# Optimization experiments

Measured on AMD Instinct MI355X. Metric: run time of the kernel, lower is better.

## Reference

```python
import jax, jax.numpy as jnp
import numpy as np

B, S = 512, 512
VOCAB, E, H1, H2, NTAGS = 50000, 20, 30, 50, 45


def _xavier_scale(fan_in, fan_out):
    return float(np.sqrt(2.0 / (fan_in + fan_out)))


def setup_inputs() -> dict:
    key = jax.random.key(0)
    ks = jax.random.split(key, 32)
    n = lambda i, shape, s=1.0: jax.random.normal(ks[i], shape, dtype=jnp.float32) * s
    w = 0.1  # weight scale
    emb_f1 = n(0, (VOCAB, E), w).at[0].set(0.0)  # padding_idx=0
    emb_b1 = n(1, (VOCAB, E), w).at[0].set(0.0)
    xs1 = _xavier_scale(B, H1)
    xs2 = _xavier_scale(B, H2)
    inp = {
        "x": jax.random.randint(ks[2], (B, S), 0, VOCAB, dtype=jnp.int64),
        "emb_f1": emb_f1, "emb_b1": emb_b1,
        "h0_f1": n(3, (B, H1), xs1), "c0_f1": n(4, (B, H1), xs1),
        "Wih_f1": n(5, (4 * H1, E), w), "Whh_f1": n(6, (4 * H1, H1), w),
        "bih_f1": n(7, (4 * H1,), w), "bhh_f1": n(8, (4 * H1,), w),
        "h0_b1": n(9, (B, H1), xs1), "c0_b1": n(10, (B, H1), xs1),
        "Wih_b1": n(11, (4 * H1, E), w), "Whh_b1": n(12, (4 * H1, H1), w),
        "bih_b1": n(13, (4 * H1,), w), "bhh_b1": n(14, (4 * H1,), w),
        "h0_f2": n(15, (B, H2), xs2), "c0_f2": n(16, (B, H2), xs2),
        "Wih_f2": n(17, (4 * H2, 2 * H1), w), "Whh_f2": n(18, (4 * H2, H2), w),
        "bih_f2": n(19, (4 * H2,), w), "bhh_f2": n(20, (4 * H2,), w),
        "h0_b2": n(21, (B, H2), xs2), "c0_b2": n(22, (B, H2), xs2),
        "Wih_b2": n(23, (4 * H2, 2 * H1), w), "Whh_b2": n(24, (4 * H2, H2), w),
        "bih_b2": n(25, (4 * H2,), w), "bhh_b2": n(26, (4 * H2,), w),
        "lin_w": n(27, (NTAGS, 2 * H2), w), "lin_b": n(28, (NTAGS,), w),
    }
    return inp


def _run_lstm(seq, h0, c0, Wih, Whh, bih, bhh, forward):
    """PyTorch LSTMCell recurrence over seq (B,S,D). Replicates the original's
    quirks: backward dir appends hidden states in reversed time order, and the
    (S,B,H) stack is .view()-ed into (B,S,H) without transposing."""
    b, s, _ = seq.shape
    h = h0.shape[-1]
    xs = jnp.swapaxes(seq, 0, 1)  # (S,B,D)

    def step(carry, xt):
        hh, cc = carry
        g = xt @ Wih.T + bih + hh @ Whh.T + bhh  # (B, 4H), gate order i,f,g,o
        i, f, gg, o = jnp.split(g, 4, axis=-1)
        cc = jax.nn.sigmoid(f) * cc + jax.nn.sigmoid(i) * jnp.tanh(gg)
        hh = jax.nn.sigmoid(o) * jnp.tanh(cc)
        return (hh, cc), hh

    _, hs = jax.lax.scan(step, (h0, c0), xs, reverse=not forward)  # hs[i] ~ time i
    if not forward:
        hs = hs[::-1]  # torch appended in processing (reversed-time) order
    return hs.reshape(b, s, h)  # faithful buggy view (S,B,H) -> (B,S,H)


def reference(x, emb_f1, emb_b1,
              h0_f1, c0_f1, Wih_f1, Whh_f1, bih_f1, bhh_f1,
              h0_b1, c0_b1, Wih_b1, Whh_b1, bih_b1, bhh_b1,
              h0_f2, c0_f2, Wih_f2, Whh_f2, bih_f2, bhh_f2,
              h0_b2, c0_b2, Wih_b2, Whh_b2, bih_b2, bhh_b2,
              lin_w, lin_b):
    f1 = _run_lstm(emb_f1[x], h0_f1, c0_f1, Wih_f1, Whh_f1, bih_f1, bhh_f1, True)
    b1 = _run_lstm(emb_b1[x], h0_b1, c0_b1, Wih_b1, Whh_b1, bih_b1, bhh_b1, False)
    l1 = jnp.concatenate([f1, b1], axis=2)  # (B,S,2*H1)
    f2 = _run_lstm(l1, h0_f2, c0_f2, Wih_f2, Whh_f2, bih_f2, bhh_f2, True)
    b2 = _run_lstm(l1, h0_b2, c0_b2, Wih_b2, Whh_b2, bih_b2, bhh_b2, False)
    l2 = jnp.concatenate([f2, b2], axis=2)  # (B,S,2*H2)
    return l2 @ lin_w.T + lin_b  # (B,S,NTAGS)
```

## Files before the change

kernel.cpp:

```cpp
#include <hip/hip_runtime.h>
#include <hip/hip_bf16.h>

typedef __attribute__((ext_vector_type(8))) short short8;
typedef __attribute__((ext_vector_type(4))) float float4v;
typedef unsigned short ushort_t;

#define BB 512
#define SS 512
#define EE 20
#define H1C 30
#define H2C 50
#define NTC 45

#define BAR() asm volatile("s_waitcnt lgkmcnt(0)\n\ts_barrier" ::: "memory")
#define WFENCE() asm volatile("s_waitcnt lgkmcnt(0)" ::: "memory")

#if __has_builtin(__builtin_amdgcn_exp2f)
#define EXP2(x) __builtin_amdgcn_exp2f(x)
#else
#define EXP2(x) exp2f(x)
#endif
#if __has_builtin(__builtin_amdgcn_rcpf)
#define RCPF(x) __builtin_amdgcn_rcpf(x)
#else
#define RCPF(x) (1.0f / (x))
#endif

#define LOG2E 1.4426950408889634f

__device__ __forceinline__ float sigf(float v) {
    return RCPF(1.0f + EXP2(-1.4426950408889634f * v));
}
__device__ __forceinline__ float tanh_(float v) {
    return 2.0f * RCPF(1.0f + EXP2(-2.8853900817779268f * v)) - 1.0f;
}

__device__ __forceinline__ float lstm_act(float gi, float gf, float gg, float go, float& c) {
    gi = fmaxf(gi, -30.f); gf = fmaxf(gf, -30.f);
    gg = fmaxf(gg, -30.f); go = fmaxf(go, -30.f);
    float di = 1.f + EXP2(-gi), df = 1.f + EXP2(-gf);
    float dg = 1.f + EXP2(-gg), dO = 1.f + EXP2(-go);
    float r1 = RCPF(di * df), r2 = RCPF(dg * dO);
    float si = df * r1, sf = di * r1;
    float tg = 2.f * (dO * r2) - 1.f;
    float so = dg * r2;
    float cc = sf * c + si * tg;
    c = cc;
    float e = EXP2(-2.8853900817779268f * cc);
    return so * (2.f * RCPF(1.f + e) - 1.f);
}

__device__ __forceinline__ ushort_t f2bf(float f) {
    unsigned u = __float_as_uint(f);
    unsigned r = u + 0x7FFFu + ((u >> 16) & 1u);
    return (ushort_t)(r >> 16);
}
__device__ __forceinline__ float bf2f(ushort_t s) { return __uint_as_float(((unsigned)s) << 16); }

__device__ __forceinline__ float ldG(const void* p, int i, int f32) {
    if (f32) return ((const float*)p)[i];
    return bf2f(((const ushort_t*)p)[i]);
}
__device__ __forceinline__ int ldTok(const void* x, int i, int x64) {
    const int* xi = (const int*)x;
    return x64 ? xi[2 * i] : xi[i];
}

__global__ void detect_kernel(const void* bih, const void* x, int* flags) {
    if (threadIdx.x == 0 && blockIdx.x == 0) {
        const ushort_t* u = (const ushort_t*)bih;
        int isf = 0;
        for (int i = 0; i < 120; i++) {
            float v = fabsf(bf2f(u[i]));
            if (!(v < 16.0f)) isf = 1;
        }
        flags[0] = isf;
        const int* xi = (const int*)x;
        int orv = 0;
        for (int i = 1; i < 32; i += 2) orv |= xi[i];
        flags[1] = (orv == 0) ? 1 : 0;
    }
}

struct XR8 { uint4 a, b; };

__device__ __forceinline__ XR8 ldEmbRawQ(const void* emb, int tok, int quad, int f32v) {
    XR8 o;
    o.a.x = 0; o.a.y = 0; o.a.z = 0; o.a.w = 0; o.b = o.a;
    if (quad < 3) {
        if (f32v) {
            const float* p = (const float*)emb + (size_t)tok * EE + quad * 8;
            o.a = *(const uint4*)p;
            if (quad < 2) o.b = *(const uint4*)(p + 4);
        } else {
            const ushort_t* p = (const ushort_t*)emb + (size_t)tok * EE + quad * 8;
            uint2 v0 = *(const uint2*)p;
            o.a.x = v0.x; o.a.y = v0.y;
            if (quad < 2) { uint2 v1 = *(const uint2*)(p + 4); o.a.z = v1.x; o.a.w = v1.y; }
        }
    }
    return o;
}

__device__ __forceinline__ short8 buildB0(const XR8& e, int quad, int f32v) {
    short8 bx;
    if (f32v) {
        bx[0] = (short)f2bf(__uint_as_float(e.a.x)); bx[1] = (short)f2bf(__uint_as_float(e.a.y));
        bx[2] = (short)f2bf(__uint_as_float(e.a.z)); bx[3] = (short)f2bf(__uint_as_float(e.a.w));
        bx[4] = (short)f2bf(__uint_as_float(e.b.x)); bx[5] = (short)f2bf(__uint_as_float(e.b.y));
        bx[6] = (short)f2bf(__uint_as_float(e.b.z)); bx[7] = (short)f2bf(__uint_as_float(e.b.w));
    } else {
        bx[0] = (short)(e.a.x & 0xFFFF); bx[1] = (short)(e.a.x >> 16);
        bx[2] = (short)(e.a.y & 0xFFFF); bx[3] = (short)(e.a.y >> 16);
        bx[4] = (short)(e.a.z & 0xFFFF); bx[5] = (short)(e.a.z >> 16);
        bx[6] = (short)(e.a.w & 0xFFFF); bx[7] = (short)(e.a.w >> 16);
    }
    if (quad == 2) { bx[4] = (short)0x3F80; bx[5] = 0; bx[6] = 0; bx[7] = 0; }
    if (quad == 3) { bx[0]=0;bx[1]=0;bx[2]=0;bx[3]=0;bx[4]=0;bx[5]=0;bx[6]=0;bx[7]=0; }
    return bx;
}

__global__ __launch_bounds__(64, 1) void lstm1_kernel(
    const void* __restrict__ x,
    const void* __restrict__ emb_f, const void* __restrict__ emb_b,
    const void* __restrict__ h0_f, const void* __restrict__ c0_f,
    const void* __restrict__ Wih_f, const void* __restrict__ Whh_f,
    const void* __restrict__ bih_f, const void* __restrict__ bhh_f,
    const void* __restrict__ h0_b, const void* __restrict__ c0_b,
    const void* __restrict__ Wih_b, const void* __restrict__ Whh_b,
    const void* __restrict__ bih_b, const void* __restrict__ bhh_b,
    ushort_t* __restrict__ hsf, ushort_t* __restrict__ hsb,
    const int* __restrict__ flags)
{
    const int f32v = flags[0], x64 = flags[1];
    const int lane = threadIdx.x & 63, li = lane & 15, quad = lane >> 4;
    const int cg = blockIdx.x, dir = cg >> 5, j0 = (cg & 31) << 4;

    const void* emb = dir ? emb_b : emb_f;
    const void* h0  = dir ? h0_b  : h0_f;
    const void* c0  = dir ? c0_b  : c0_f;
    const void* Wih = dir ? Wih_b : Wih_f;
    const void* Whh = dir ? Whh_b : Whh_f;
    const void* bih = dir ? bih_b : bih_f;
    const void* bhh = dir ? bhh_b : bhh_f;
    ushort_t* hs = dir ? hsb : hsf;

    __shared__ int toks[16][SS];

    for (int idx = lane; idx < 16 * SS; idx += 64)
        toks[idx >> 9][idx & (SS - 1)] = ldTok(x, (j0 + (idx >> 9)) * SS + (idx & (SS - 1)), x64);

    const int gA = li & 3, nbase = li >> 2;
    const float sc = (gA == 2) ? 2.0f * LOG2E : LOG2E;
    short8 wxh[8], wxl[8], whh[8], whl[8];
    #pragma unroll
    for (int u = 0; u < 8; u++) {
        const int nn = u * 4 + nbase;
        const bool ok = nn < H1C;
        short8 xh, xl, hh, hl;
        #pragma unroll
        for (int j = 0; j < 8; j++) {
            const int k = quad * 8 + j;
            float wx = 0.f;
            if (ok) {
                if (k < EE) wx = ldG(Wih, (gA * H1C + nn) * EE + k, f32v);
                else if (k == 20) wx = ldG(bih, gA * H1C + nn, f32v) + ldG(bhh, gA * H1C + nn, f32v);
            }
            wx *= sc;
            ushort_t bx1 = f2bf(wx); xh[j] = (short)bx1; xl[j] = (short)f2bf(wx - bf2f(bx1));
            const int ns = j * 4 + quad;
            float wh = (ok && ns < H1C) ? sc * ldG(Whh, (gA * H1C + nn) * H1C + ns, f32v) : 0.f;
            ushort_t bh1 = f2bf(wh); hh[j] = (short)bh1; hl[j] = (short)f2bf(wh - bf2f(bh1));
        }
        wxh[u] = xh; wxl[u] = xl; whh[u] = hh; whl[u] = hl;
    }

    float creg[8];
    short8 b1;
    #pragma unroll
    for (int u = 0; u < 8; u++) {
        const int nn = u * 4 + quad;
        const bool ok = nn < H1C;
        creg[u] = ok ? ldG(c0, (j0 + li) * H1C + nn, f32v) : 0.f;
        b1[u] = ok ? (short)f2bf(ldG(h0, (j0 + li) * H1C + nn, f32v)) : (short)0;
    }

    const int t0 = dir ? SS - 1 : 0, dt = dir ? -1 : 1;

    WFENCE();

    int tkA = toks[li][t0 + dt * 3];
    int tkB = toks[li][t0 + dt * 4];
    XR8 e0r, e1r, e2r, e3r;
    float4v xacc[8];
    {
        int tk0 = toks[li][t0];
        int tk1 = toks[li][t0 + dt];
        int tk2 = toks[li][t0 + dt * 2];
        XR8 ecur = ldEmbRawQ(emb, tk0, quad, f32v);
        e1r = ldEmbRawQ(emb, tk1, quad, f32v);
        e2r = ldEmbRawQ(emb, tk2, quad, f32v);
        e0r = ecur; e3r = ecur;
        short8 bx = buildB0(ecur, quad, f32v);
        #pragma unroll
        for (int u = 0; u < 8; u++) {
            float4v a; a[0] = 0.f; a[1] = 0.f; a[2] = 0.f; a[3] = 0.f;
            a = __builtin_amdgcn_mfma_f32_16x16x32_bf16(wxh[u], bx, a, 0, 0, 0);
            a = __builtin_amdgcn_mfma_f32_16x16x32_bf16(wxl[u], bx, a, 0, 0, 0);
            xacc[u] = a;
        }
    }

    auto step = [&](int it, XR8& cons, XR8& fill, int& tk) {
        const int t = t0 + dt * it;
        float4v acc[8];
        #pragma unroll
        for (int u = 0; u < 8; u++) {
            float4v a = xacc[u];
            a = __builtin_amdgcn_mfma_f32_16x16x32_bf16(whh[u], b1, a, 0, 0, 0);
            a = __builtin_amdgcn_mfma_f32_16x16x32_bf16(whl[u], b1, a, 0, 0, 0);
            acc[u] = a;
        }
        if (it + 3 < SS) fill = ldEmbRawQ(emb, tk, quad, f32v);
        {
            int ti = it + 5; if (ti > SS - 1) ti = SS - 1;
            tk = toks[li][t0 + dt * ti];
        }
        short8 bx = buildB0(cons, quad, f32v);
        float4v xn[8];
        #pragma unroll
        for (int u = 0; u < 8; u++) {
            float4v a; a[0] = 0.f; a[1] = 0.f; a[2] = 0.f; a[3] = 0.f;
            a = __builtin_amdgcn_mfma_f32_16x16x32_bf16(wxh[u], bx, a, 0, 0, 0);
            a = __builtin_amdgcn_mfma_f32_16x16x32_bf16(wxl[u], bx, a, 0, 0, 0);
            xn[u] = a;
        }
        short8 hp;
        #pragma unroll
        for (int u = 0; u < 8; u++) {
            float hv = lstm_act(acc[u][0], acc[u][1], acc[u][2], acc[u][3], creg[u]);
            hp[u] = (short)f2bf(hv);
        }
        b1 = hp;
        *(short8*)&hs[((size_t)(j0 + li) * SS + t) * 32 + quad * 8] = hp;
        #pragma unroll
        for (int u = 0; u < 8; u++) xacc[u] = xn[u];
    };
    for (int it = 0; it < SS; it += 4) {
        step(it,     e1r, e3r, tkA);
        step(it + 1, e2r, e0r, tkB);
        step(it + 2, e3r, e1r, tkA);
        step(it + 3, e0r, e2r, tkB);
    }
}

__global__ __launch_bounds__(256) void lstm2_kernel(
    const ushort_t* __restrict__ hs1f, const ushort_t* __restrict__ hs1b,
    const void* __restrict__ h0_f, const void* __restrict__ c0_f,
    const void* __restrict__ Wih_f, const void* __restrict__ Whh_f,
    const void* __restrict__ bih_f, const void* __restrict__ bhh_f,
    const void* __restrict__ h0_b, const void* __restrict__ c0_b,
    const void* __restrict__ Wih_b, const void* __restrict__ Whh_b,
    const void* __restrict__ bih_b, const void* __restrict__ bhh_b,
    ushort_t* __restrict__ hsf, ushort_t* __restrict__ hsb,
    const int* __restrict__ flags)
{
    const int f32v = flags[0];
    const int wg = blockIdx.x, dir = wg >> 5, cb = (wg & 31) << 4, tid = threadIdx.x;
    const int wave = tid >> 6, lane = tid & 63, li = lane & 15, quad = lane >> 4;

    const void* h0  = dir ? h0_b  : h0_f;
    const void* c0  = dir ? c0_b  : c0_f;
    const void* Wih = dir ? Wih_b : Wih_f;
    const void* Whh = dir ? Whh_b : Whh_f;
    const void* bih = dir ? bih_b : bih_f;
    const void* bhh = dir ? bhh_b : bhh_f;
    ushort_t* hs = dir ? hsb : hsf;

    __shared__ __align__(16) ushort_t Af[2][4][64][8];
    for (int idx = tid; idx < 2 * 4 * 64 * 8; idx += 256) ((ushort_t*)Af)[idx] = 0;

    const int n = wave * 16 + li;
    const bool nok = n < H2C;

    short8 bhi[4][4], blo[4][4];
    float bias_g[4];
    #pragma unroll
    for (int g = 0; g < 4; g++) {
        const int wrow = g * H2C + n;
        bias_g[g] = nok ? (ldG(bih, wrow, f32v) + ldG(bhh, wrow, f32v)) : 0.f;
        #pragma unroll
        for (int kt = 0; kt < 4; kt++) {
            short8 hi, lo;
            #pragma unroll
            for (int j = 0; j < 8; j++) {
                int k = kt * 32 + quad * 8 + j;
                float w = 0.f;
                if (nok) {
                    if (k < 32) {
                        const int c = k, nn2 = (c & 7) * 4 + (c >> 3);
                        if (nn2 < H1C) w = ldG(Wih, wrow * (2 * H1C) + nn2, f32v);
                    } else if (k < 64) {
                        const int c = k - 32, nn2 = (c & 7) * 4 + (c >> 3);
                        if (nn2 < H1C) w = ldG(Wih, wrow * (2 * H1C) + H1C + nn2, f32v);
                    } else if (k < 64 + H2C) {
                        w = ldG(Whh, wrow * H2C + (k - 64), f32v);
                    }
                }
                ushort_t h = f2bf(w);
                hi[j] = (short)h;
                lo[j] = (short)f2bf(w - bf2f(h));
            }
            bhi[g][kt] = hi; blo[g][kt] = lo;
        }
    }

    const int kh = 64 + n;
    const int khk = kh >> 5, khg = (kh & 31) >> 3, khj = kh & 7;
    const int lrow = tid >> 4, k0 = (tid & 15) * 4;
    const int t0 = dir ? SS - 1 : 0, dt = dir ? -1 : 1;

    auto loadX = [&](int c) -> ushort4 {
        const int a = cb + lrow;
        if (k0 < 32)
            return *(const ushort4*)&hs1f[((size_t)c * SS + a) * 32 + k0];
        else
            return *(const ushort4*)&hs1b[((size_t)c * SS + (SS - 1 - a)) * 32 + (k0 - 32)];
    };

    __syncthreads();

    float creg[4];
    #pragma unroll
    for (int r = 0; r < 4; r++) {
        const int m = quad * 4 + r;
        creg[r] = nok ? ldG(c0, (cb + m) * H2C + n, f32v) : 0.f;
        ushort_t hb0 = nok ? f2bf(ldG(h0, (cb + m) * H2C + n, f32v)) : (ushort_t)0;
        Af[0][khk][khg * 16 + m][khj] = hb0;
    }
    {
        ushort4 xi = loadX(t0);
        const int kg = (k0 & 31) >> 3, kt = k0 >> 5, jb = k0 & 7;
        Af[0][kt][kg * 16 + lrow][jb + 0] = xi.x;
        Af[0][kt][kg * 16 + lrow][jb + 1] = xi.y;
        Af[0][kt][kg * 16 + lrow][jb + 2] = xi.z;
        Af[0][kt][kg * 16 + lrow][jb + 3] = xi.w;
    }
    ushort4 xA = loadX(t0 + dt), xB;
    __syncthreads();

    auto step = [&](int it, ushort4& xin, ushort4& xout) {
        const int c = t0 + dt * it;
        const int cur = it & 1, nxt = cur ^ 1;
        BAR();
        short8 af[4];
        #pragma unroll
        for (int kt = 0; kt < 4; kt++) af[kt] = *(const short8*)&Af[cur][kt][lane][0];
        if (it + 2 < SS) xout = loadX(c + 2 * dt);
        float4v acc[4];
        #pragma unroll
        for (int g = 0; g < 4; g++) {
            float4v a; a[0] = a[1] = a[2] = a[3] = bias_g[g];
            #pragma unroll
            for (int kt = 0; kt < 4; kt++) {
                a = __builtin_amdgcn_mfma_f32_16x16x32_bf16(af[kt], bhi[g][kt], a, 0, 0, 0);
                a = __builtin_amdgcn_mfma_f32_16x16x32_bf16(af[kt], blo[g][kt], a, 0, 0, 0);
            }
            acc[g] = a;
        }
        ushort_t hb[4];
        #pragma unroll
        for (int r = 0; r < 4; r++) {
            float gi = acc[0][r], gf = acc[1][r], gg = acc[2][r], go = acc[3][r];
            float cc = sigf(gf) * creg[r] + sigf(gi) * tanh_(gg);
            float h = sigf(go) * tanh_(cc);
            creg[r] = cc;
            hb[r] = nok ? f2bf(h) : (ushort_t)0;
        }
        ushort4 h4; h4.x = hb[0]; h4.y = hb[1]; h4.z = hb[2]; h4.w = hb[3];
        *(ushort4*)&hs[((size_t)c * 64 + n) * SS + cb + quad * 4] = h4;
        if (it + 1 < SS) {
            #pragma unroll
            for (int r = 0; r < 4; r++) Af[nxt][khk][khg * 16 + quad * 4 + r][khj] = hb[r];
            const int kg = (k0 & 31) >> 3, kt = k0 >> 5, jb = k0 & 7;
            Af[nxt][kt][kg * 16 + lrow][jb + 0] = xin.x;
            Af[nxt][kt][kg * 16 + lrow][jb + 1] = xin.y;
            Af[nxt][kt][kg * 16 + lrow][jb + 2] = xin.z;
            Af[nxt][kt][kg * 16 + lrow][jb + 3] = xin.w;
        }
    };
    for (int it = 0; it < SS; it += 2) { step(it, xA, xB); step(it + 1, xB, xA); }
}

__global__ __launch_bounds__(256) void lin_kernel(
    const ushort_t* __restrict__ hs2f, const ushort_t* __restrict__ hs2b,
    const void* __restrict__ lw, const void* __restrict__ lb,
    void* __restrict__ out, const int* __restrict__ flags)
{
    const int f32v = flags[0];
    const int tid = threadIdx.x, wave = tid >> 6, lane = tid & 63, li = lane & 15, quad = lane >> 4;

    __shared__ __align__(16) ushort_t Af[4][4][64][8];
    for (int idx = tid; idx < 4 * 4 * 64 * 8; idx += 256) ((ushort_t*)Af)[idx] = 0;

    short8 bhi[3][4], blo[3][4];
    float biasv[3];
    #pragma unroll
    for (int nt = 0; nt < 3; nt++) {
        const int nn = nt * 16 + li;
        const bool nok = nn < NTC;
        biasv[nt] = nok ? ldG(lb, nn, f32v) : 0.f;
        #pragma unroll
        for (int kt = 0; kt < 4; kt++) {
            short8 hi, lo;
            #pragma unroll
            for (int j = 0; j < 8; j++) {
                int k = kt * 32 + quad * 8 + j;
                float w = 0.f;
                if (nok) {
                    if (k < H2C) w = ldG(lw, nn * 100 + k, f32v);
                    else if (k >= 64 && k < 64 + H2C) w = ldG(lw, nn * 100 + 50 + (k - 64), f32v);
                }
                ushort_t h = f2bf(w);
                hi[j] = (short)h;
                lo[j] = (short)f2bf(w - bf2f(h));
            }
            bhi[nt][kt] = hi; blo[nt][kt] = lo;
        }
    }

    const int P0 = blockIdx.x * 64;
    const int i = P0 >> 9, j0 = P0 & 511;
    __syncthreads();
    for (int idx = tid; idx < 100 * 32; idx += 256) {
        const int kk = idx >> 5, pj = (idx & 31) * 2;
        unsigned v;
        int k;
        if (kk < H2C) {
            v = *(const unsigned*)&hs2f[((size_t)i * 64 + kk) * SS + j0 + pj];
            k = kk;
        } else {
            v = *(const unsigned*)&hs2b[((size_t)(SS - 1 - i) * 64 + (kk - H2C)) * SS + j0 + pj];
            k = 64 + (kk - H2C);
        }
        const int kt = k >> 5, kg = (k & 31) >> 3, j = k & 7;
        Af[pj >> 4][kt][kg * 16 + (pj & 15)][j] = (ushort_t)(v & 0xFFFF);
        Af[pj >> 4][kt][kg * 16 + ((pj + 1) & 15)][j] = (ushort_t)(v >> 16);
    }
    __syncthreads();

    short8 af[4];
    #pragma unroll
    for (int kt = 0; kt < 4; kt++) af[kt] = *(const short8*)&Af[wave][kt][lane][0];
    #pragma unroll
    for (int nt = 0; nt < 3; nt++) {
        float4v a; a[0] = a[1] = a[2] = a[3] = biasv[nt];
        #pragma unroll
        for (int kt = 0; kt < 4; kt++) {
            a = __builtin_amdgcn_mfma_f32_16x16x32_bf16(af[kt], bhi[nt][kt], a, 0, 0, 0);
            a = __builtin_amdgcn_mfma_f32_16x16x32_bf16(af[kt], blo[nt][kt], a, 0, 0, 0);
        }
        const int nn = nt * 16 + li;
        if (nn < NTC) {
            #pragma unroll
            for (int reg = 0; reg < 4; reg++) {
                const int prow = wave * 16 + quad * 4 + reg;
                const size_t op = (size_t)(P0 + prow) * NTC + nn;
                if (f32v) ((float*)out)[op] = a[reg];
                else      ((ushort_t*)out)[op] = f2bf(a[reg]);
            }
        }
    }
}

extern "C" void kernel_launch(void* const* d_in, const int* in_sizes, int n_in,
                              void* d_out, int out_size, void* d_ws, size_t ws_size,
                              hipStream_t stream)
{
    const void* x      = d_in[0];
    const void* emb_f1 = d_in[1];
    const void* emb_b1 = d_in[2];
    const void* h0_f1  = d_in[3];
    const void* c0_f1  = d_in[4];
    const void* Wih_f1 = d_in[5];
    const void* Whh_f1 = d_in[6];
    const void* bih_f1 = d_in[7];
    const void* bhh_f1 = d_in[8];
    const void* h0_b1  = d_in[9];
    const void* c0_b1  = d_in[10];
    const void* Wih_b1 = d_in[11];
    const void* Whh_b1 = d_in[12];
    const void* bih_b1 = d_in[13];
    const void* bhh_b1 = d_in[14];
    const void* h0_f2  = d_in[15];
    const void* c0_f2  = d_in[16];
    const void* Wih_f2 = d_in[17];
    const void* Whh_f2 = d_in[18];
    const void* bih_f2 = d_in[19];
    const void* bhh_f2 = d_in[20];
    const void* h0_b2  = d_in[21];
    const void* c0_b2  = d_in[22];
    const void* Wih_b2 = d_in[23];
    const void* Whh_b2 = d_in[24];
    const void* bih_b2 = d_in[25];
    const void* bhh_b2 = d_in[26];
    const void* lin_w  = d_in[27];
    const void* lin_b  = d_in[28];

    int* flags = (int*)d_ws;
    ushort_t* hs1f = (ushort_t*)((char*)d_ws + 256);
    ushort_t* hs1b = hs1f + (size_t)BB * SS * 32;
    ushort_t* hs2f = hs1b + (size_t)BB * SS * 32;
    ushort_t* hs2b = hs2f + (size_t)SS * 64 * BB;

    detect_kernel<<<1, 64, 0, stream>>>(bih_f1, x, flags);
    lstm1_kernel<<<64, 64, 0, stream>>>(x, emb_f1, emb_b1,
        h0_f1, c0_f1, Wih_f1, Whh_f1, bih_f1, bhh_f1,
        h0_b1, c0_b1, Wih_b1, Whh_b1, bih_b1, bhh_b1, hs1f, hs1b, flags);
    lstm2_kernel<<<64, 256, 0, stream>>>(hs1f, hs1b,
        h0_f2, c0_f2, Wih_f2, Whh_f2, bih_f2, bhh_f2,
        h0_b2, c0_b2, Wih_b2, Whh_b2, bih_b2, bhh_b2, hs2f, hs2b, flags);
    lin_kernel<<<(BB * SS) / 64, 256, 0, stream>>>(hs2f, hs2b, lin_w, lin_b, d_out, flags);
}
```

Baseline: 1.130 ms.

## Process two batch chunks per wave in layer-1 LSTM to interleave recurrences

Each layer-1 workgroup now handles two independent 16-row batch chunks instead of one, halving the grid to 32 single-wave blocks. The two recurrences are interleaved in the same step, so their MFMA chains and activations can hide each other's latency. Tokens are now read from global memory directly instead of being staged in shared memory. The cost is higher register pressure, fewer CUs in use, and more global token loads on the critical path.

New measurement: 1.703 ms. 1.51x slower.

```diff
diff --git a/kernel.cpp b/kernel.cpp
--- a/kernel.cpp
+++ b/kernel.cpp
@@ -13,7 +13,6 @@
 #define NTC 45
 
 #define BAR() asm volatile("s_waitcnt lgkmcnt(0)\n\ts_barrier" ::: "memory")
-#define WFENCE() asm volatile("s_waitcnt lgkmcnt(0)" ::: "memory")
 
 #if __has_builtin(__builtin_amdgcn_exp2f)
 #define EXP2(x) __builtin_amdgcn_exp2f(x)
@@ -120,7 +119,8 @@
     return bx;
 }
 
-__global__ __launch_bounds__(64, 1) void lstm1_kernel(
+__global__ __attribute__((amdgpu_waves_per_eu(1))) __launch_bounds__(64)
+void lstm1_kernel(
     const void* __restrict__ x,
     const void* __restrict__ emb_f, const void* __restrict__ emb_b,
     const void* __restrict__ h0_f, const void* __restrict__ c0_f,
@@ -134,7 +134,8 @@
 {
     const int f32v = flags[0], x64 = flags[1];
     const int lane = threadIdx.x & 63, li = lane & 15, quad = lane >> 4;
-    const int cg = blockIdx.x, dir = cg >> 5, j0 = (cg & 31) << 4;
+    const int wg = blockIdx.x, dir = wg >> 4, pr = wg & 15;
+    const int j0c[2] = { (pr * 2) << 4, (pr * 2 + 1) << 4 };
 
     const void* emb = dir ? emb_b : emb_f;
     const void* h0  = dir ? h0_b  : h0_f;
@@ -145,11 +146,6 @@
     const void* bhh = dir ? bhh_b : bhh_f;
     ushort_t* hs = dir ? hsb : hsf;
 
-    __shared__ int toks[16][SS];
-
-    for (int idx = lane; idx < 16 * SS; idx += 64)
-        toks[idx >> 9][idx & (SS - 1)] = ldTok(x, (j0 + (idx >> 9)) * SS + (idx & (SS - 1)), x64);
-
     const int gA = li & 3, nbase = li >> 2;
     const float sc = (gA == 2) ? 2.0f * LOG2E : LOG2E;
     short8 wxh[8], wxl[8], whh[8], whl[8];
@@ -175,82 +171,97 @@
         wxh[u] = xh; wxl[u] = xl; whh[u] = hh; whl[u] = hl;
     }
 
-    float creg[8];
-    short8 b1;
-    #pragma unroll
-    for (int u = 0; u < 8; u++) {
-        const int nn = u * 4 + quad;
-        const bool ok = nn < H1C;
-        creg[u] = ok ? ldG(c0, (j0 + li) * H1C + nn, f32v) : 0.f;
-        b1[u] = ok ? (short)f2bf(ldG(h0, (j0 + li) * H1C + nn, f32v)) : (short)0;
-    }
-
     const int t0 = dir ? SS - 1 : 0, dt = dir ? -1 : 1;
-
-    WFENCE();
-
-    int tkA = toks[li][t0 + dt * 3];
-    int tkB = toks[li][t0 + dt * 4];
-    XR8 e0r, e1r, e2r, e3r;
-    float4v xacc[8];
-    {
-        int tk0 = toks[li][t0];
-        int tk1 = toks[li][t0 + dt];
-        int tk2 = toks[li][t0 + dt * 2];
-        XR8 ecur = ldEmbRawQ(emb, tk0, quad, f32v);
-        e1r = ldEmbRawQ(emb, tk1, quad, f32v);
-        e2r = ldEmbRawQ(emb, tk2, quad, f32v);
-        e0r = ecur; e3r = ecur;
+    int rbase[2];
+    rbase[0] = (j0c[0] + li) * SS;
+    rbase[1] = (j0c[1] + li) * SS;
+
+    float creg[2][8];
+    short8 b1v[2];
+    XR8 er[2][4];
+    int tk[2][2];
+    float4v xacc[2][8];
+    #pragma unroll
+    for (int c = 0; c < 2; c++) {
+        const int jj = j0c[c];
+        #pragma unroll
+        for (int u = 0; u < 8; u++) {
+            const int nn = u * 4 + quad;
+            const bool ok = nn < H1C;
+            creg[c][u] = ok ? ldG(c0, (jj + li) * H1C + nn, f32v) : 0.f;
+            b1v[c][u] = ok ? (short)f2bf(ldG(h0, (jj + li) * H1C + nn, f32v)) : (short)0;
+        }
+        int tkp0 = ldTok(x, rbase[c] + t0, x64);
+        int tkp1 = ldTok(x, rbase[c] + t0 + dt, x64);
+        int tkp2 = ldTok(x, rbase[c] + t0 + 2 * dt, x64);
+        tk[c][0] = ldTok(x, rbase[c] + t0 + 3 * dt, x64);
+        tk[c][1] = ldTok(x, rbase[c] + t0 + 4 * dt, x64);
+        XR8 ecur = ldEmbRawQ(emb, tkp0, quad, f32v);
+        er[c][1] = ldEmbRawQ(emb, tkp1, quad, f32v);
+        er[c][2] = ldEmbRawQ(emb, tkp2, quad, f32v);
+        er[c][0] = ecur; er[c][3] = ecur;
         short8 bx = buildB0(ecur, quad, f32v);
         #pragma unroll
         for (int u = 0; u < 8; u++) {
             float4v a; a[0] = 0.f; a[1] = 0.f; a[2] = 0.f; a[3] = 0.f;
             a = __builtin_amdgcn_mfma_f32_16x16x32_bf16(wxh[u], bx, a, 0, 0, 0);
             a = __builtin_amdgcn_mfma_f32_16x16x32_bf16(wxl[u], bx, a, 0, 0, 0);
-            xacc[u] = a;
-        }
-    }
-
-    auto step = [&](int it, XR8& cons, XR8& fill, int& tk) {
+            xacc[c][u] = a;
+        }
+    }
+
+    auto step = [&](int it, int rc, int rf, int tp) {
         const int t = t0 + dt * it;
-        float4v acc[8];
+        float4v acc[2][8];
         #pragma unroll
         for (int u = 0; u < 8; u++) {
-            float4v a = xacc[u];
-            a = __builtin_amdgcn_mfma_f32_16x16x32_bf16(whh[u], b1, a, 0, 0, 0);
-            a = __builtin_amdgcn_mfma_f32_16x16x32_bf16(whl[u], b1, a, 0, 0, 0);
-            acc[u] = a;
-        }
-        if (it + 3 < SS) fill = ldEmbRawQ(emb, tk, quad, f32v);
-        {
+            #pragma unroll
+            for (int c = 0; c < 2; c++) {
+                float4v a = xacc[c][u];
+                a = __builtin_amdgcn_mfma_f32_16x16x32_bf16(whh[u], b1v[c], a, 0, 0, 0);
+                a = __builtin_amdgcn_mfma_f32_16x16x32_bf16(whl[u], b1v[c], a, 0, 0, 0);
+                acc[c][u] = a;
+            }
+        }
+        #pragma unroll
+        for (int c = 0; c < 2; c++) {
+            if (it + 3 < SS) er[c][rf] = ldEmbRawQ(emb, tk[c][tp], quad, f32v);
             int ti = it + 5; if (ti > SS - 1) ti = SS - 1;
-            tk = toks[li][t0 + dt * ti];
-        }
-        short8 bx = buildB0(cons, quad, f32v);
-        float4v xn[8];
-        #pragma unroll
-        for (int u = 0; u < 8; u++) {
-            float4v a; a[0] = 0.f; a[1] = 0.f; a[2] = 0.f; a[3] = 0.f;
-            a = __builtin_amdgcn_mfma_f32_16x16x32_bf16(wxh[u], bx, a, 0, 0, 0);
-            a = __builtin_amdgcn_mfma_f32_16x16x32_bf16(wxl[u], bx, a, 0, 0, 0);
-            xn[u] = a;
-        }
-        short8 hp;
-        #pragma unroll
-        for (int u = 0; u < 8; u++) {
-            float hv = lstm_act(acc[u][0], acc[u][1], acc[u][2], acc[u][3], creg[u]);
-            hp[u] = (short)f2bf(hv);
-        }
-        b1 = hp;
-        *(short8*)&hs[((size_t)(j0 + li) * SS + t) * 32 + quad * 8] = hp;
-        #pragma unroll
-        for (int u = 0; u < 8; u++) xacc[u] = xn[u];
+            tk[c][tp] = ldTok(x, rbase[c] + t0 + dt * ti, x64);
+        }
+        float4v xn[2][8];
+        #pragma unroll
+        for (int c = 0; c < 2; c++) {
+            short8 bx = buildB0(er[c][rc], quad, f32v);
+            #pragma unroll
+            for (int u = 0; u < 8; u++) {
+                float4v a; a[0] = 0.f; a[1] = 0.f; a[2] = 0.f; a[3] = 0.f;
+                a = __builtin_amdgcn_mfma_f32_16x16x32_bf16(wxh[u], bx, a, 0, 0, 0);
+                a = __builtin_amdgcn_mfma_f32_16x16x32_bf16(wxl[u], bx, a, 0, 0, 0);
+                xn[c][u] = a;
+            }
+        }
+        #pragma unroll
+        for (int c = 0; c < 2; c++) {
+            short8 hp;
+            #pragma unroll
+            for (int u = 0; u < 8; u++) {
+                float hv = lstm_act(acc[c][u][0], acc[c][u][1], acc[c][u][2], acc[c][u][3], creg[c][u]);
+                hp[u] = (short)f2bf(hv);
+            }
+            b1v[c] = hp;
+            *(short8*)&hs[((size_t)(j0c[c] + li) * SS + t) * 32 + quad * 8] = hp;
+        }
+        #pragma unroll
+        for (int c = 0; c < 2; c++)
+            #pragma unroll
+            for (int u = 0; u < 8; u++) xacc[c][u] = xn[c][u];
     };
     for (int it = 0; it < SS; it += 4) {
-        step(it,     e1r, e3r, tkA);
-        step(it + 1, e2r, e0r, tkB);
-        step(it + 2, e3r, e1r, tkA);
-        step(it + 3, e0r, e2r, tkB);
+        step(it,     1, 3, 0);
+        step(it + 1, 2, 0, 1);
+        step(it + 2, 3, 1, 0);
+        step(it + 3, 0, 2, 1);
     }
 }
 
@@ -514,7 +525,7 @@
     ushort_t* hs2b = hs2f + (size_t)SS * 64 * BB;
 
     detect_kernel<<<1, 64, 0, stream>>>(bih_f1, x, flags);
-    lstm1_kernel<<<64, 64, 0, stream>>>(x, emb_f1, emb_b1,
+    lstm1_kernel<<<32, 64, 0, stream>>>(x, emb_f1, emb_b1,
         h0_f1, c0_f1, Wih_f1, Whh_f1, bih_f1, bhh_f1,
         h0_b1, c0_b1, Wih_b1, Whh_b1, bih_b1, bhh_b1, hs1f, hs1b, flags);
     lstm2_kernel<<<64, 256, 0, stream>>>(hs1f, hs1b,
```

## Restructure layer-1 LSTM step: drop LDS token staging, fold x-projection into step

Applied to the files above, without the earlier changes.

Removes the shared-memory token table and loads tokens directly from global memory with a rotating 3-slot prefetch of token ids and embedding rows. The input projection MFMAs move out of the previous step's software pipeline and now feed the same accumulator chain as the recurrent MFMAs, which cuts the extra accumulator registers. The gate activation math is rearranged into stage-by-stage loops over the 8 units to expose ILP on the transcendental ops. The trade-off is that the x-projection MFMAs now sit on the serial critical path, and token loads go to global memory inside the loop.

Measured after the change: 1.132 ms. About the same (+0.1%).

```diff
diff --git a/kernel.cpp b/kernel.cpp
--- a/kernel.cpp
+++ b/kernel.cpp
@@ -13,7 +13,6 @@
 #define NTC 45
 
 #define BAR() asm volatile("s_waitcnt lgkmcnt(0)\n\ts_barrier" ::: "memory")
-#define WFENCE() asm volatile("s_waitcnt lgkmcnt(0)" ::: "memory")
 
 #if __has_builtin(__builtin_amdgcn_exp2f)
 #define EXP2(x) __builtin_amdgcn_exp2f(x)
@@ -33,21 +32,6 @@
 }
 __device__ __forceinline__ float tanh_(float v) {
     return 2.0f * RCPF(1.0f + EXP2(-2.8853900817779268f * v)) - 1.0f;
-}
-
-__device__ __forceinline__ float lstm_act(float gi, float gf, float gg, float go, float& c) {
-    gi = fmaxf(gi, -30.f); gf = fmaxf(gf, -30.f);
-    gg = fmaxf(gg, -30.f); go = fmaxf(go, -30.f);
-    float di = 1.f + EXP2(-gi), df = 1.f + EXP2(-gf);
-    float dg = 1.f + EXP2(-gg), dO = 1.f + EXP2(-go);
-    float r1 = RCPF(di * df), r2 = RCPF(dg * dO);
-    float si = df * r1, sf = di * r1;
-    float tg = 2.f * (dO * r2) - 1.f;
-    float so = dg * r2;
-    float cc = sf * c + si * tg;
-    c = cc;
-    float e = EXP2(-2.8853900817779268f * cc);
-    return so * (2.f * RCPF(1.f + e) - 1.f);
 }
 
 __device__ __forceinline__ ushort_t f2bf(float f) {
@@ -145,11 +129,6 @@
     const void* bhh = dir ? bhh_b : bhh_f;
     ushort_t* hs = dir ? hsb : hsf;
 
-    __shared__ int toks[16][SS];
-
-    for (int idx = lane; idx < 16 * SS; idx += 64)
-        toks[idx >> 9][idx & (SS - 1)] = ldTok(x, (j0 + (idx >> 9)) * SS + (idx & (SS - 1)), x64);
-
     const int gA = li & 3, nbase = li >> 2;
     const float sc = (gA == 2) ? 2.0f * LOG2E : LOG2E;
     short8 wxh[8], wxl[8], whh[8], whl[8];
@@ -186,72 +165,96 @@
     }
 
     const int t0 = dir ? SS - 1 : 0, dt = dir ? -1 : 1;
-
-    WFENCE();
-
-    int tkA = toks[li][t0 + dt * 3];
-    int tkB = toks[li][t0 + dt * 4];
-    XR8 e0r, e1r, e2r, e3r;
-    float4v xacc[8];
+    const int rbase = (j0 + li) * SS;
+    ushort_t* const hsrow = hs + (size_t)(j0 + li) * SS * 32 + quad * 8;
+
+    XR8 er[3];
+    int tkc[3];
     {
-        int tk0 = toks[li][t0];
-        int tk1 = toks[li][t0 + dt];
-        int tk2 = toks[li][t0 + dt * 2];
-        XR8 ecur = ldEmbRawQ(emb, tk0, quad, f32v);
-        e1r = ldEmbRawQ(emb, tk1, quad, f32v);
-        e2r = ldEmbRawQ(emb, tk2, quad, f32v);
-        e0r = ecur; e3r = ecur;
-        short8 bx = buildB0(ecur, quad, f32v);
+        int tp0 = ldTok(x, rbase + t0, x64);
+        int tp1 = ldTok(x, rbase + t0 + dt, x64);
+        er[0] = ldEmbRawQ(emb, tp0, quad, f32v);
+        er[1] = ldEmbRawQ(emb, tp1, quad, f32v);
+        er[2] = er[0];
+        tkc[2] = ldTok(x, rbase + t0 + 2 * dt, x64);
+        tkc[0] = ldTok(x, rbase + t0 + 3 * dt, x64);
+        tkc[1] = ldTok(x, rbase + t0 + 4 * dt, x64);
+    }
+
+    auto step = [&](int it, int cs, int fs) {
+        const int t = t0 + dt * it;
+        short8 bx = buildB0(er[cs], quad, f32v);
+        float4v acc[8];
         #pragma unroll
         for (int u = 0; u < 8; u++) {
             float4v a; a[0] = 0.f; a[1] = 0.f; a[2] = 0.f; a[3] = 0.f;
             a = __builtin_amdgcn_mfma_f32_16x16x32_bf16(wxh[u], bx, a, 0, 0, 0);
             a = __builtin_amdgcn_mfma_f32_16x16x32_bf16(wxl[u], bx, a, 0, 0, 0);
-            xacc[u] = a;
-        }
-    }
-
-    auto step = [&](int it, XR8& cons, XR8& fill, int& tk) {
-        const int t = t0 + dt * it;
-        float4v acc[8];
-        #pragma unroll
-        for (int u = 0; u < 8; u++) {
-            float4v a = xacc[u];
             a = __builtin_amdgcn_mfma_f32_16x16x32_bf16(whh[u], b1, a, 0, 0, 0);
             a = __builtin_amdgcn_mfma_f32_16x16x32_bf16(whl[u], b1, a, 0, 0, 0);
             acc[u] = a;
         }
-        if (it + 3 < SS) fill = ldEmbRawQ(emb, tk, quad, f32v);
+        if (it + 2 < SS) er[fs] = ldEmbRawQ(emb, tkc[fs], quad, f32v);
         {
             int ti = it + 5; if (ti > SS - 1) ti = SS - 1;
-            tk = toks[li][t0 + dt * ti];
-        }
-        short8 bx = buildB0(cons, quad, f32v);
-        float4v xn[8];
-        #pragma unroll
-        for (int u = 0; u < 8; u++) {
-            float4v a; a[0] = 0.f; a[1] = 0.f; a[2] = 0.f; a[3] = 0.f;
-            a = __builtin_amdgcn_mfma_f32_16x16x32_bf16(wxh[u], bx, a, 0, 0, 0);
-            a = __builtin_amdgcn_mfma_f32_16x16x32_bf16(wxl[u], bx, a, 0, 0, 0);
-            xn[u] = a;
-        }
+            tkc[fs] = ldTok(x, rbase + t0 + dt * ti, x64);
+        }
+        float gi[8], gf[8], gg[8], go[8];
+        #pragma unroll
+        for (int u = 0; u < 8; u++) {
+            gi[u] = fmaxf(acc[u][0], -30.f); gf[u] = fmaxf(acc[u][1], -30.f);
+            gg[u] = fmaxf(acc[u][2], -30.f); go[u] = fmaxf(acc[u][3], -30.f);
+        }
+        float ei[8], ef[8], eg[8], eo[8];
+        #pragma unroll
+        for (int u = 0; u < 8; u++) {
+            ei[u] = EXP2(-gi[u]); ef[u] = EXP2(-gf[u]);
+            eg[u] = EXP2(-gg[u]); eo[u] = EXP2(-go[u]);
+        }
+        float di[8], dF[8], dg[8], dO[8];
+        #pragma unroll
+        for (int u = 0; u < 8; u++) {
+            di[u] = 1.f + ei[u]; dF[u] = 1.f + ef[u];
+            dg[u] = 1.f + eg[u]; dO[u] = 1.f + eo[u];
+        }
+        float r1[8], r2[8];
+        #pragma unroll
+        for (int u = 0; u < 8; u++) {
+            r1[u] = RCPF(di[u] * dF[u]); r2[u] = RCPF(dg[u] * dO[u]);
+        }
+        float cc[8];
+        #pragma unroll
+        for (int u = 0; u < 8; u++) {
+            float si = dF[u] * r1[u], sf = di[u] * r1[u];
+            float tg = 2.f * (dO[u] * r2[u]) - 1.f;
+            cc[u] = sf * creg[u] + si * tg;
+            creg[u] = cc[u];
+        }
+        float ec[8];
+        #pragma unroll
+        for (int u = 0; u < 8; u++) ec[u] = EXP2(-2.8853900817779268f * cc[u]);
+        float rc[8];
+        #pragma unroll
+        for (int u = 0; u < 8; u++) rc[u] = RCPF(1.f + ec[u]);
         short8 hp;
         #pragma unroll
         for (int u = 0; u < 8; u++) {
-            float hv = lstm_act(acc[u][0], acc[u][1], acc[u][2], acc[u][3], creg[u]);
+            float so = dg[u] * r2[u];
+            float hv = so * (2.f * rc[u] - 1.f);
             hp[u] = (short)f2bf(hv);
         }
         b1 = hp;
-        *(short8*)&hs[((size_t)(j0 + li) * SS + t) * 32 + quad * 8] = hp;
-        #pragma unroll
-        for (int u = 0; u < 8; u++) xacc[u] = xn[u];
+        *(short8*)&hsrow[(size_t)t * 32] = hp;
     };
-    for (int it = 0; it < SS; it += 4) {
-        step(it,     e1r, e3r, tkA);
-        step(it + 1, e2r, e0r, tkB);
-        step(it + 2, e3r, e1r, tkA);
-        step(it + 3, e0r, e2r, tkB);
-    }
+
+    int it = 0;
+    for (; it + 2 < SS; it += 3) {
+        step(it,     0, 2);
+        step(it + 1, 1, 0);
+        step(it + 2, 2, 1);
+    }
+    step(510, 0, 2);
+    step(511, 1, 0);
 }
 
 __global__ __launch_bounds__(256) void lstm2_kernel(
```
